# Optimization experiments

Hardware: AMD Instinct MI355X
Metric: run time of the kernel (lower is better)

Reference implementation:

```python
import jax, jax.numpy as jnp
import numpy as np

I = 512  # input_size
H = 512  # hidden_size
B = 16384  # batch


def setup_inputs() -> dict:
    key = jax.random.key(0)
    ks = jax.random.split(key, 8)
    s_g = 1.0 / np.sqrt(I + H)
    s_i = 1.0 / np.sqrt(I)
    s_h = 1.0 / np.sqrt(H)
    return {
        "input": jax.random.normal(ks[0], (B, I), dtype=jnp.float32),
        "hidden": jax.random.normal(ks[1], (B, H), dtype=jnp.float32),
        "W_gate": jax.random.uniform(ks[2], (2 * H, I + H), minval=-s_g, maxval=s_g, dtype=jnp.float32),
        "b_gate": jax.random.uniform(ks[3], (2 * H,), minval=-s_g, maxval=s_g, dtype=jnp.float32),
        "W_i": jax.random.uniform(ks[4], (H, I), minval=-s_i, maxval=s_i, dtype=jnp.float32),
        "b_i": jax.random.uniform(ks[5], (H,), minval=-s_i, maxval=s_i, dtype=jnp.float32),
        "W_h": jax.random.uniform(ks[6], (H, H), minval=-s_h, maxval=s_h, dtype=jnp.float32),
        "b_h": jax.random.uniform(ks[7], (H,), minval=-s_h, maxval=s_h, dtype=jnp.float32),
    }


def reference(input, hidden, W_gate, b_gate, W_i, b_i, W_h, b_h):
    # combined linear for r/z gates: [B, I+H] @ [I+H, 2H]
    combined = jnp.concatenate([input, hidden], axis=1)
    gates = combined @ W_gate.T + b_gate  # [B, 2H]
    r_gate = jax.nn.sigmoid(gates[:, :H])
    z_gate = jax.nn.sigmoid(gates[:, H:])
    i_gate = input @ W_i.T + b_i   # [B, H]
    h_gate = hidden @ W_h.T + b_h  # [B, H]
    n_gate = jnp.tanh(i_gate + r_gate * h_gate)
    new_hidden = (1.0 - z_gate) * n_gate + z_gate * hidden
    return new_hidden  # dropout p=0.0 -> identity
```

## Files before the change

### kernel.cpp

```cpp
#include <hip/hip_runtime.h>
#include <cstdint>
#include <cstddef>


typedef __attribute__((ext_vector_type(8))) __bf16 bf16x8;
typedef __attribute__((ext_vector_type(4))) float f32x4;
typedef __attribute__((ext_vector_type(8))) unsigned short u16x8;

__device__ __forceinline__ unsigned short f2bf(float f) {
    unsigned u = __builtin_bit_cast(unsigned, f);
    return (unsigned short)((u + 0x7fffu + ((u >> 16) & 1u)) >> 16);
}

__global__ void prep_x(const float* __restrict__ inp, const float* __restrict__ hid,
                       unsigned short* __restrict__ X) {
    int t = blockIdx.x * 256 + threadIdx.x;
    int b = t >> 7;
    int j = (t & 127) << 3;
    const float* src = (j < 512) ? (inp + (size_t)b * 512 + j)
                                 : (hid + (size_t)b * 512 + (j - 512));
    u16x8 o;
#pragma unroll
    for (int e = 0; e < 8; ++e) o[e] = f2bf(src[e]);
    *reinterpret_cast<u16x8*>(X + (size_t)b * 1024 + j) = o;
}

__global__ void prep_w(const float* __restrict__ Wg, const float* __restrict__ Wi,
                       const float* __restrict__ Wh,
                       unsigned short* __restrict__ Wrz, unsigned short* __restrict__ Wih) {
    int t = blockIdx.x * 256 + threadIdx.x;
    if (t < 131072) {
        const float* src = Wg + (size_t)t * 8;
        u16x8 o;
#pragma unroll
        for (int e = 0; e < 8; ++e) o[e] = f2bf(src[e]);
        *reinterpret_cast<u16x8*>(Wrz + (size_t)t * 8) = o;
    } else {
        int u = t - 131072;
        int n = u >> 7;
        int k = (u & 127) << 3;
        const float* src = (k < 512) ? (Wi + (size_t)n * 512 + k)
                                     : (Wh + (size_t)n * 512 + (k - 512));
        u16x8 o;
#pragma unroll
        for (int e = 0; e < 8; ++e) o[e] = f2bf(src[e]);
        *reinterpret_cast<u16x8*>(Wih + (size_t)n * 1024 + k) = o;
    }
}

__device__ __forceinline__ void gload16(const void* g, void* l) {
    __builtin_amdgcn_global_load_lds(
        (const __attribute__((address_space(1))) void*)g,
        (__attribute__((address_space(3))) void*)l, 16, 0, 0);
}

__device__ __forceinline__ bf16x8 ldfrag32(const unsigned short* base, int row, int c0) {
    const char* p = (const char*)base + row * 64 + ((c0 ^ ((row >> 1) & 3)) << 4);
    return *reinterpret_cast<const bf16x8*>(p);
}

__global__ __launch_bounds__(256, 2) void gru_fused(
        const unsigned short* __restrict__ X,
        const unsigned short* __restrict__ Wr,
        const unsigned short* __restrict__ Wz,
        const unsigned short* __restrict__ Wih,
        const float* __restrict__ hid,
        const float* __restrict__ bgate,
        const float* __restrict__ bi,
        const float* __restrict__ bh,
        float* __restrict__ out) {
    __shared__ unsigned short lds[2][10240];

    const int tid = threadIdx.x;
    const int lane = tid & 63;
    const int wid = tid >> 6;
    const int wm = wid >> 1, wn = wid & 1;
    const int bid = blockIdx.x;
    const int bn = bid & 7;
    const int bm = bid >> 3;

    const int srow = tid >> 2;
    const int lc = (tid & 3) ^ ((tid >> 3) & 3);
    const char* gX0 = (const char*)X   + ((size_t)(bm * 128 + srow) * 1024 + lc * 8) * 2;
    const char* gX1 = gX0 + 64 * 2048;
    const char* gR  = (const char*)Wr  + ((size_t)(bn * 64 + srow) * 1024 + lc * 8) * 2;
    const char* gZ  = (const char*)Wz  + ((size_t)(bn * 64 + srow) * 1024 + lc * 8) * 2;
    const char* gW  = (const char*)Wih + ((size_t)(bn * 64 + srow) * 1024 + lc * 8) * 2;

    f32x4 accR[4][2], accZ[4][2], accI[4][2], accH[4][2];
#pragma unroll
    for (int i = 0; i < 4; ++i)
#pragma unroll
        for (int j = 0; j < 2; ++j) {
            accR[i][j] = (f32x4){0.f, 0.f, 0.f, 0.f};
            accZ[i][j] = (f32x4){0.f, 0.f, 0.f, 0.f};
            accI[i][j] = (f32x4){0.f, 0.f, 0.f, 0.f};
            accH[i][j] = (f32x4){0.f, 0.f, 0.f, 0.f};
        }

    const int ra = wm * 64 + (lane & 15);
    const int rb = wn * 32 + (lane & 15);
    const int c0 = lane >> 4;

#define STAGE(t, b) {                                                  \
        gload16(gX0 + (t) * 64, (char*)lds[b] + tid * 16);             \
        gload16(gX1 + (t) * 64, (char*)lds[b] + 4096 + tid * 16);      \
        gload16(gR  + (t) * 64, (char*)lds[b] + 8192 + tid * 16);      \
        gload16(gZ  + (t) * 64, (char*)lds[b] + 12288 + tid * 16);     \
        gload16(gW  + (t) * 64, (char*)lds[b] + 16384 + tid * 16); }

#define MFMA8(ACC, B0, B1)                                                            \
    ACC[0][0] = __builtin_amdgcn_mfma_f32_16x16x32_bf16(a0, B0, ACC[0][0], 0, 0, 0); \
    ACC[1][0] = __builtin_amdgcn_mfma_f32_16x16x32_bf16(a1, B0, ACC[1][0], 0, 0, 0); \
    ACC[2][0] = __builtin_amdgcn_mfma_f32_16x16x32_bf16(a2, B0, ACC[2][0], 0, 0, 0); \
    ACC[3][0] = __builtin_amdgcn_mfma_f32_16x16x32_bf16(a3, B0, ACC[3][0], 0, 0, 0); \
    ACC[0][1] = __builtin_amdgcn_mfma_f32_16x16x32_bf16(a0, B1, ACC[0][1], 0, 0, 0); \
    ACC[1][1] = __builtin_amdgcn_mfma_f32_16x16x32_bf16(a1, B1, ACC[1][1], 0, 0, 0); \
    ACC[2][1] = __builtin_amdgcn_mfma_f32_16x16x32_bf16(a2, B1, ACC[2][1], 0, 0, 0); \
    ACC[3][1] = __builtin_amdgcn_mfma_f32_16x16x32_bf16(a3, B1, ACC[3][1], 0, 0, 0);

#define COMPUTE(b, ACC3) {                                             \
        const unsigned short* bp = lds[b];                             \
        bf16x8 a0 = ldfrag32(bp, ra,      c0);                         \
        bf16x8 a1 = ldfrag32(bp, ra + 16, c0);                         \
        bf16x8 a2 = ldfrag32(bp, ra + 32, c0);                         \
        bf16x8 a3 = ldfrag32(bp, ra + 48, c0);                         \
        bf16x8 b0 = ldfrag32(bp + 4096, rb, c0);                       \
        bf16x8 b1 = ldfrag32(bp + 4096, rb + 16, c0);                  \
        MFMA8(accR, b0, b1)                                            \
        b0 = ldfrag32(bp + 6144, rb, c0);                              \
        b1 = ldfrag32(bp + 6144, rb + 16, c0);                         \
        MFMA8(accZ, b0, b1)                                            \
        b0 = ldfrag32(bp + 8192, rb, c0);                              \
        b1 = ldfrag32(bp + 8192, rb + 16, c0);                         \
        MFMA8(ACC3, b0, b1) }

    STAGE(0, 0)
    __syncthreads();

#pragma unroll 2
    for (int t = 0; t < 16; ++t) {
        STAGE(t + 1, (t + 1) & 1)
        COMPUTE(t & 1, accI)
        __syncthreads();
    }
#pragma unroll 2
    for (int t = 16; t < 32; ++t) {
        if (t < 31) STAGE(t + 1, (t + 1) & 1)
        COMPUTE(t & 1, accH)
        __syncthreads();
    }
#undef COMPUTE
#undef MFMA8
#undef STAGE

    const int colb = bn * 64 + wn * 32 + (lane & 15);
    const int rowb = bm * 128 + wm * 64 + ((lane >> 4) << 2);
#pragma unroll
    for (int ni = 0; ni < 2; ++ni) {
        const int n = colb + ni * 16;
        const float bgr = bgate[n];
        const float bgz = bgate[512 + n];
        const float bii = bi[n];
        const float bhh = bh[n];
#pragma unroll
        for (int mi = 0; mi < 4; ++mi) {
#pragma unroll
            for (int r = 0; r < 4; ++r) {
                const int m = rowb + mi * 16 + r;
                const size_t off = (size_t)m * 512 + n;
                float rg = accR[mi][ni][r] + bgr;
                rg = 1.f / (1.f + __expf(-rg));
                float zg = accZ[mi][ni][r] + bgz;
                zg = 1.f / (1.f + __expf(-zg));
                float x = accI[mi][ni][r] + bii + rg * (accH[mi][ni][r] + bhh);
                x = fminf(fmaxf(x, -15.f), 15.f);
                const float e = __expf(2.f * x);
                const float ng = (e - 1.f) / (e + 1.f);
                out[off] = ng + zg * (hid[off] - ng);
            }
        }
    }
}

extern "C" void kernel_launch(void* const* d_in, const int* in_sizes, int n_in,
                              void* d_out, int out_size, void* d_ws, size_t ws_size,
                              hipStream_t stream) {
    const float* inp = (const float*)d_in[0];
    const float* hid = (const float*)d_in[1];
    const float* Wg  = (const float*)d_in[2];
    const float* bg  = (const float*)d_in[3];
    const float* Wi  = (const float*)d_in[4];
    const float* bi  = (const float*)d_in[5];
    const float* Wh  = (const float*)d_in[6];
    const float* bh  = (const float*)d_in[7];
    float* out = (float*)d_out;

    unsigned short* X   = (unsigned short*)d_ws;
    unsigned short* Wrz = (unsigned short*)((char*)d_ws + 33554432);
    unsigned short* Wih = (unsigned short*)((char*)d_ws + 33554432 + 2097152);

    prep_x<<<8192, 256, 0, stream>>>(inp, hid, X);
    prep_w<<<768, 256, 0, stream>>>(Wg, Wi, Wh, Wrz, Wih);
    gru_fused<<<1024, 256, 0, stream>>>(X, Wrz, Wrz + 512 * 1024, Wih,
                                        hid, bg, bi, bh, out);
}
```

Baseline: 185.4 us.

## Triple-buffer LDS tiles with explicit vmcnt waits and raw barriers

```diff
diff --git a/kernel.cpp b/kernel.cpp
--- a/kernel.cpp
+++ b/kernel.cpp
@@ -58,6 +58,9 @@
     const char* p = (const char*)base + row * 64 + ((c0 ^ ((row >> 1) & 3)) << 4);
     return *reinterpret_cast<const bf16x8*>(p);
 }
+
+#define WAITV(n) asm volatile("s_waitcnt vmcnt(" #n ")" ::: "memory")
+#define FENCE()  asm volatile("" ::: "memory")
 
 __global__ __launch_bounds__(256, 2) void gru_fused(
         const unsigned short* __restrict__ X,
@@ -69,7 +72,7 @@
         const float* __restrict__ bi,
         const float* __restrict__ bh,
         float* __restrict__ out) {
-    __shared__ unsigned short lds[2][10240];
+    __shared__ unsigned short lds[3][10240];
 
     const int tid = threadIdx.x;
     const int lane = tid & 63;
@@ -103,11 +106,12 @@
     const int c0 = lane >> 4;
 
 #define STAGE(t, b) {                                                  \
-        gload16(gX0 + (t) * 64, (char*)lds[b] + tid * 16);             \
-        gload16(gX1 + (t) * 64, (char*)lds[b] + 4096 + tid * 16);      \
-        gload16(gR  + (t) * 64, (char*)lds[b] + 8192 + tid * 16);      \
-        gload16(gZ  + (t) * 64, (char*)lds[b] + 12288 + tid * 16);     \
-        gload16(gW  + (t) * 64, (char*)lds[b] + 16384 + tid * 16); }
+        char* lp = (char*)lds[b] + tid * 16;                           \
+        gload16(gX0 + (t) * 64, lp);                                   \
+        gload16(gX1 + (t) * 64, lp + 4096);                            \
+        gload16(gR  + (t) * 64, lp + 8192);                            \
+        gload16(gZ  + (t) * 64, lp + 12288);                           \
+        gload16(gW  + (t) * 64, lp + 16384); }
 
 #define MFMA8(ACC, B0, B1)                                                            \
     ACC[0][0] = __builtin_amdgcn_mfma_f32_16x16x32_bf16(a0, B0, ACC[0][0], 0, 0, 0); \
@@ -135,21 +139,35 @@
         b1 = ldfrag32(bp + 8192, rb + 16, c0);                         \
         MFMA8(ACC3, b0, b1) }
 
+#define PIPE(t) {                                                      \
+        __builtin_amdgcn_s_barrier();  \
+        FENCE();                                                       \
+        if ((t) + 3 < 32) STAGE((t) + 3, (t) % 3)                      \
+        if ((t) < 29)       { WAITV(10); }                             \
+        else if ((t) == 29) { WAITV(5); }                              \
+        else                { WAITV(0); }                              \
+        __builtin_amdgcn_s_barrier();    \
+        FENCE();                                                       \
+    }
+
     STAGE(0, 0)
-    __syncthreads();
-
-#pragma unroll 2
+    STAGE(1, 1)
+    STAGE(2, 2)
+    WAITV(10);
+    __builtin_amdgcn_s_barrier();
+    FENCE();
+
+#pragma unroll 1
     for (int t = 0; t < 16; ++t) {
-        STAGE(t + 1, (t + 1) & 1)
-        COMPUTE(t & 1, accI)
-        __syncthreads();
-    }
-#pragma unroll 2
+        COMPUTE(t % 3, accI)
+        PIPE(t)
+    }
+#pragma unroll 1
     for (int t = 16; t < 32; ++t) {
-        if (t < 31) STAGE(t + 1, (t + 1) & 1)
-        COMPUTE(t & 1, accH)
-        __syncthreads();
-    }
+        COMPUTE(t % 3, accH)
+        if (t < 31) PIPE(t)
+    }
+#undef PIPE
 #undef COMPUTE
 #undef MFMA8
 #undef STAGE
```

New measurement: 186.7 us. About the same (+0.7%).
